# Kernel optimization log

Measured on AMD Instinct MI355X. Metric: run time of the kernel, lower is better.

The kernel has to match this reference:

```python
import jax, jax.numpy as jnp
import numpy as np

HIDDEN = 512
MEM = 512
COMM = 512
N = 8192


def setup_inputs() -> dict:
    key = jax.random.key(0)
    ks = jax.random.split(key, 8)
    in_dim = HIDDEN + MEM
    s = 1.0 / np.sqrt(in_dim)
    return {
        "u": jax.random.normal(ks[0], (N, HIDDEN), dtype=jnp.float32),
        "z": jax.random.normal(ks[1], (N, MEM), dtype=jnp.float32),
        # torch Linear weights have shape (out, in); biases init to 0 per _init_weights
        "Wk": jax.random.normal(ks[2], (COMM, in_dim), dtype=jnp.float32) * s,
        "bk": jnp.zeros((COMM,), dtype=jnp.float32),
        "Wv": jax.random.normal(ks[3], (COMM, in_dim), dtype=jnp.float32) * s,
        "bv": jnp.zeros((COMM,), dtype=jnp.float32),
        "Wq": jax.random.normal(ks[4], (COMM, in_dim), dtype=jnp.float32) * s,
        "bq": jnp.zeros((COMM,), dtype=jnp.float32),
    }


def reference(u, z, Wk, bk, Wv, bv, Wq, bq):
    n = u.shape[0]
    scale = jnp.sqrt(jnp.asarray(Wk.shape[0], dtype=u.dtype))
    s = jnp.concatenate([u, z], axis=-1)              # (N, in_dim)
    keys = s @ Wk.T + bk                              # (N, C)
    values = s @ Wv.T + bv                            # (N, C)
    queries = s @ Wq.T + bq                           # (N, C)
    scores = (queries @ keys.T) / scale               # (N, N)
    eye = jnp.eye(n, dtype=bool)
    scores = jnp.where(eye, -jnp.inf, scores)         # self-mask
    comm_attn = jax.nn.softmax(scores, axis=-1)
    comm_attn = jnp.nan_to_num(comm_attn, nan=0.0)
    m_bar = comm_attn @ values                        # (N, C)
    return (m_bar, comm_attn)
```

## Files before the change

### kernel.cpp

```cpp
#include <hip/hip_runtime.h>
#include <hip/hip_bf16.h>
#include <stdint.h>

#define N_TOK 8192
#define IN_DIM 1024
#define CDIM 512
#define NW 1536

typedef short bf16x8 __attribute__((ext_vector_type(8)));
typedef float f32x4 __attribute__((ext_vector_type(4)));

__device__ __forceinline__ unsigned short f2bf(float f) {
  union { float f; unsigned int u; } x; x.f = f;
  unsigned int u = x.u;
  u += 0x7fffu + ((u >> 16) & 1u);
  return (unsigned short)(u >> 16);
}
__device__ __forceinline__ float bf2f(unsigned short us) {
  union { unsigned int u; float f; } x; x.u = ((unsigned int)us) << 16;
  return x.f;
}

#define GLD16(g, l) __builtin_amdgcn_global_load_lds( \
    (const __attribute__((address_space(1))) void*)(g), \
    (__attribute__((address_space(3))) void*)(l), 16, 0, 0)

__global__ __launch_bounds__(256) void k_convert(
    const float* __restrict__ u, const float* __restrict__ z,
    const float* __restrict__ wk, const float* __restrict__ wv,
    const float* __restrict__ wq,
    ushort* __restrict__ Sb, ushort* __restrict__ Wb) {
  const int S4 = N_TOK * IN_DIM / 4;
  const int W4 = NW * IN_DIM / 4;
  const int total = S4 + W4;
  for (int e = blockIdx.x * blockDim.x + threadIdx.x; e < total;
       e += gridDim.x * blockDim.x) {
    float4 v; ushort* dst;
    if (e < S4) {
      int idx = e << 2; int row = idx >> 10; int col = idx & 1023;
      const float* src = (col < 512) ? (u + row * 512 + col)
                                     : (z + row * 512 + (col - 512));
      v = *(const float4*)src;
      dst = Sb + idx;
    } else {
      int idx = (e - S4) << 2; int row = idx >> 10; int col = idx & 1023;
      const float* base = (row < 512) ? wk : (row < 1024 ? wv : wq);
      v = *(const float4*)(base + (size_t)(row & 511) * 1024 + col);
      dst = Wb + idx;
    }
    ushort4 o;
    o.x = f2bf(v.x); o.y = f2bf(v.y); o.z = f2bf(v.z); o.w = f2bf(v.w);
    *(ushort4*)dst = o;
  }
}

__global__ __launch_bounds__(256) void k_kvq(
    const ushort* __restrict__ Sb, const ushort* __restrict__ Wb,
    const float* __restrict__ bk, const float* __restrict__ bv,
    const float* __restrict__ bq,
    ushort* __restrict__ Kb, ushort* __restrict__ Qb, ushort* __restrict__ VT) {
  __shared__ __align__(16) ushort As[128 * 64];
  __shared__ __align__(16) ushort Bs[128 * 64];
  const int tid = threadIdx.x, lane = tid & 63, w = tid >> 6;
  const int wr = w >> 1, wc = w & 1;
  const int tm = blockIdx.x, tn = blockIdx.y;

  f32x4 acc[4][4];
#pragma unroll
  for (int m = 0; m < 4; m++)
#pragma unroll
    for (int n = 0; n < 4; n++) acc[m][n] = (f32x4){0.f, 0.f, 0.f, 0.f};

  const ushort* ga0 = Sb + (size_t)tm * 128 * IN_DIM;
  const ushort* gb0 = Wb + (size_t)tn * 128 * IN_DIM;

  for (int k0 = 0; k0 < IN_DIM; k0 += 64) {
#pragma unroll
    for (int i = 0; i < 4; i++) {
      int ce = i * 256 + tid;
      int row = ce >> 3, c8 = (ce & 7) << 3;
      GLD16(ga0 + (size_t)row * IN_DIM + k0 + c8, As + ce * 8);
      GLD16(gb0 + (size_t)row * IN_DIM + k0 + c8, Bs + ce * 8);
    }
    __syncthreads();
#pragma unroll
    for (int kb = 0; kb < 2; kb++) {
      bf16x8 af[4], bfr[4];
#pragma unroll
      for (int m = 0; m < 4; m++)
        af[m] = *(const bf16x8*)(As + (wr * 64 + m * 16 + (lane & 15)) * 64 +
                                 kb * 32 + ((lane >> 4) << 3));
#pragma unroll
      for (int n = 0; n < 4; n++)
        bfr[n] = *(const bf16x8*)(Bs + (wc * 64 + n * 16 + (lane & 15)) * 64 +
                                  kb * 32 + ((lane >> 4) << 3));
#pragma unroll
      for (int m = 0; m < 4; m++)
#pragma unroll
        for (int n = 0; n < 4; n++)
          acc[m][n] = __builtin_amdgcn_mfma_f32_16x16x32_bf16(af[m], bfr[n],
                                                              acc[m][n], 0, 0, 0);
    }
    __syncthreads();
  }

  const int region = tn >> 2;
  const int colr = (tn & 3) * 128 + wc * 64;
  const int rbase = tm * 128 + wr * 64;
  const float* bias = (region == 0) ? bk : (region == 1 ? bv : bq);
  if (region == 1) {
#pragma unroll
    for (int m = 0; m < 4; m++) {
      int r0 = rbase + m * 16 + ((lane >> 4) << 2);
#pragma unroll
      for (int n = 0; n < 4; n++) {
        int c = colr + n * 16 + (lane & 15);
        float b = bias[c];
        ushort4 pk;
        pk.x = f2bf(acc[m][n][0] + b);
        pk.y = f2bf(acc[m][n][1] + b);
        pk.z = f2bf(acc[m][n][2] + b);
        pk.w = f2bf(acc[m][n][3] + b);
        *(ushort4*)(VT + (size_t)c * N_TOK + r0) = pk;
      }
    }
  } else {
    ushort* O = (region == 0) ? Kb : Qb;
#pragma unroll
    for (int m = 0; m < 4; m++) {
      int r0 = rbase + m * 16 + ((lane >> 4) << 2);
#pragma unroll
      for (int n = 0; n < 4; n++) {
        int c = colr + n * 16 + (lane & 15);
        float b = bias[c];
#pragma unroll
        for (int rg = 0; rg < 4; rg++)
          O[(size_t)(r0 + rg) * CDIM + c] = f2bf(acc[m][n][rg] + b);
      }
    }
  }
}

__global__ __launch_bounds__(256) void k_scores(
    const ushort* __restrict__ Qb, const ushort* __restrict__ Kb,
    ushort* __restrict__ E, float* __restrict__ rowpart) {
  __shared__ __align__(16) ushort As[128 * 64];
  __shared__ __align__(16) ushort Bs[128 * 64];
  __shared__ float sums[256];
  const int tid = threadIdx.x, lane = tid & 63, w = tid >> 6;
  const int wr = w >> 1, wc = w & 1;
  const int tm = blockIdx.x, tn = blockIdx.y;

  f32x4 acc[4][4];
#pragma unroll
  for (int m = 0; m < 4; m++)
#pragma unroll
    for (int n = 0; n < 4; n++) acc[m][n] = (f32x4){0.f, 0.f, 0.f, 0.f};

  const ushort* ga0 = Qb + (size_t)tm * 128 * CDIM;
  const ushort* gb0 = Kb + (size_t)tn * 128 * CDIM;

  for (int k0 = 0; k0 < CDIM; k0 += 64) {
#pragma unroll
    for (int i = 0; i < 4; i++) {
      int ce = i * 256 + tid;
      int row = ce >> 3, c8 = (ce & 7) << 3;
      GLD16(ga0 + (size_t)row * CDIM + k0 + c8, As + ce * 8);
      GLD16(gb0 + (size_t)row * CDIM + k0 + c8, Bs + ce * 8);
    }
    __syncthreads();
#pragma unroll
    for (int kb = 0; kb < 2; kb++) {
      bf16x8 af[4], bfr[4];
#pragma unroll
      for (int m = 0; m < 4; m++)
        af[m] = *(const bf16x8*)(As + (wr * 64 + m * 16 + (lane & 15)) * 64 +
                                 kb * 32 + ((lane >> 4) << 3));
#pragma unroll
      for (int n = 0; n < 4; n++)
        bfr[n] = *(const bf16x8*)(Bs + (wc * 64 + n * 16 + (lane & 15)) * 64 +
                                  kb * 32 + ((lane >> 4) << 3));
#pragma unroll
      for (int m = 0; m < 4; m++)
#pragma unroll
        for (int n = 0; n < 4; n++)
          acc[m][n] = __builtin_amdgcn_mfma_f32_16x16x32_bf16(af[m], bfr[n],
                                                              acc[m][n], 0, 0, 0);
    }
    __syncthreads();
  }

  const float scale = 0.044194173824159216f;
  float rs[4][4];
#pragma unroll
  for (int m = 0; m < 4; m++)
#pragma unroll
    for (int rg = 0; rg < 4; rg++) rs[m][rg] = 0.f;

#pragma unroll
  for (int m = 0; m < 4; m++) {
    int grow_b = tm * 128 + wr * 64 + m * 16 + ((lane >> 4) << 2);
#pragma unroll
    for (int n = 0; n < 4; n++) {
      int gcol = tn * 128 + wc * 64 + n * 16 + (lane & 15);
#pragma unroll
      for (int rg = 0; rg < 4; rg++) {
        int grow = grow_b + rg;
        float ev = (grow == gcol) ? 0.0f : __expf(acc[m][n][rg] * scale);
        unsigned short evb = f2bf(ev);
        E[(size_t)grow * N_TOK + gcol] = evb;
        rs[m][rg] += bf2f(evb);
      }
    }
  }
#pragma unroll
  for (int m = 0; m < 4; m++)
#pragma unroll
    for (int rg = 0; rg < 4; rg++) {
      float s = rs[m][rg];
      s += __shfl_xor(s, 1);
      s += __shfl_xor(s, 2);
      s += __shfl_xor(s, 4);
      s += __shfl_xor(s, 8);
      rs[m][rg] = s;
    }
  if ((lane & 15) == 0) {
#pragma unroll
    for (int m = 0; m < 4; m++)
#pragma unroll
      for (int rg = 0; rg < 4; rg++)
        sums[wc * 128 + wr * 64 + m * 16 + ((lane >> 4) << 2) + rg] = rs[m][rg];
  }
  __syncthreads();
  if (tid < 128)
    rowpart[(size_t)(tm * 128 + tid) * 64 + tn] = sums[tid] + sums[128 + tid];
}

__global__ __launch_bounds__(256) void k_rcp(const float* __restrict__ rowpart,
                                             float* __restrict__ rcp_l) {
  int row = blockIdx.x * blockDim.x + threadIdx.x;
  if (row < N_TOK) {
    const float4* p = (const float4*)(rowpart + (size_t)row * 64);
    float s = 0.f;
#pragma unroll
    for (int i = 0; i < 16; i++) {
      float4 v = p[i];
      s += v.x + v.y + v.z + v.w;
    }
    rcp_l[row] = 1.0f / s;
  }
}

__global__ __launch_bounds__(256) void k_pv_norm(
    const ushort* __restrict__ E, const ushort* __restrict__ VT,
    const float* __restrict__ rcp_l, float* __restrict__ mbar,
    float* __restrict__ attn) {
  __shared__ __align__(16) ushort As[128 * 64];
  __shared__ __align__(16) ushort Bs[64 * 64];
  const int tid = threadIdx.x, lane = tid & 63, w = tid >> 6;
  const int wr = w >> 1, wc = w & 1;
  const int tm = blockIdx.x, tn = blockIdx.y;

  f32x4 acc[4][2];
#pragma unroll
  for (int m = 0; m < 4; m++)
#pragma unroll
    for (int n = 0; n < 2; n++) acc[m][n] = (f32x4){0.f, 0.f, 0.f, 0.f};

  const ushort* ga0 = E + (size_t)tm * 128 * N_TOK;
  const ushort* gb0 = VT + (size_t)tn * 64 * N_TOK;
  const int kw_lo = tn << 10;
  const int kw_hi = kw_lo + 1024;

  for (int k0 = 0; k0 < N_TOK; k0 += 64) {
#pragma unroll
    for (int i = 0; i < 4; i++) {
      int ce = i * 256 + tid;
      int row = ce >> 3, c8 = (ce & 7) << 3;
      GLD16(ga0 + (size_t)row * N_TOK + k0 + c8, As + ce * 8);
    }
#pragma unroll
    for (int i = 0; i < 2; i++) {
      int ce = i * 256 + tid;
      int row = ce >> 3, c8 = (ce & 7) << 3;
      GLD16(gb0 + (size_t)row * N_TOK + k0 + c8, Bs + ce * 8);
    }
    __syncthreads();
#pragma unroll
    for (int kb = 0; kb < 2; kb++) {
      bf16x8 af[4], bfr[2];
#pragma unroll
      for (int m = 0; m < 4; m++)
        af[m] = *(const bf16x8*)(As + (wr * 64 + m * 16 + (lane & 15)) * 64 +
                                 kb * 32 + ((lane >> 4) << 3));
#pragma unroll
      for (int n = 0; n < 2; n++)
        bfr[n] = *(const bf16x8*)(Bs + (wc * 32 + n * 16 + (lane & 15)) * 64 +
                                  kb * 32 + ((lane >> 4) << 3));
#pragma unroll
      for (int m = 0; m < 4; m++)
#pragma unroll
        for (int n = 0; n < 2; n++)
          acc[m][n] = __builtin_amdgcn_mfma_f32_16x16x32_bf16(af[m], bfr[n],
                                                              acc[m][n], 0, 0, 0);
    }

    if (attn != nullptr && k0 >= kw_lo && k0 < kw_hi) {
#pragma unroll
      for (int p = 0; p < 4; p++) {
        int ce = p * 256 + tid;
        int row = ce >> 3;
        int c8 = (ce & 7) << 3;
        int grow = tm * 128 + row;
        float rl = rcp_l[grow];
        uint4 ev = *(const uint4*)(E + ((size_t)grow << 13) + k0 + c8);
        float4 o0, o1;
        o0.x = bf2f((unsigned short)(ev.x & 0xffffu)) * rl;
        o0.y = bf2f((unsigned short)(ev.x >> 16)) * rl;
        o0.z = bf2f((unsigned short)(ev.y & 0xffffu)) * rl;
        o0.w = bf2f((unsigned short)(ev.y >> 16)) * rl;
        o1.x = bf2f((unsigned short)(ev.z & 0xffffu)) * rl;
        o1.y = bf2f((unsigned short)(ev.z >> 16)) * rl;
        o1.z = bf2f((unsigned short)(ev.w & 0xffffu)) * rl;
        o1.w = bf2f((unsigned short)(ev.w >> 16)) * rl;
        float* op = attn + ((size_t)grow << 13) + k0 + c8;
        *(float4*)op = o0;
        *(float4*)(op + 4) = o1;
      }
    }
    __syncthreads();
  }

#pragma unroll
  for (int m = 0; m < 4; m++) {
    int r0 = tm * 128 + wr * 64 + m * 16 + ((lane >> 4) << 2);
#pragma unroll
    for (int n = 0; n < 2; n++) {
      int c = tn * 64 + wc * 32 + n * 16 + (lane & 15);
#pragma unroll
      for (int rg = 0; rg < 4; rg++)
        mbar[(size_t)(r0 + rg) * CDIM + c] = acc[m][n][rg] * rcp_l[r0 + rg];
    }
  }
}

__global__ __launch_bounds__(256) void k_norm(
    const ushort* __restrict__ E, float* __restrict__ attn,
    const float* __restrict__ rcp_l, int row0, int nrows) {
  const int units = nrows << 10;
  for (int uidx = blockIdx.x * blockDim.x + threadIdx.x; uidx < units;
       uidx += gridDim.x * blockDim.x) {
    int row = row0 + (uidx >> 10);
    int c8 = (uidx & 1023) << 3;
    const float rl = rcp_l[row];
    uint4 ev = *(const uint4*)(E + ((size_t)row << 13) + c8);
    float4 o0, o1;
    o0.x = bf2f((unsigned short)(ev.x & 0xffffu)) * rl;
    o0.y = bf2f((unsigned short)(ev.x >> 16)) * rl;
    o0.z = bf2f((unsigned short)(ev.y & 0xffffu)) * rl;
    o0.w = bf2f((unsigned short)(ev.y >> 16)) * rl;
    o1.x = bf2f((unsigned short)(ev.z & 0xffffu)) * rl;
    o1.y = bf2f((unsigned short)(ev.z >> 16)) * rl;
    o1.z = bf2f((unsigned short)(ev.w & 0xffffu)) * rl;
    o1.w = bf2f((unsigned short)(ev.w >> 16)) * rl;
    float* op = attn + ((size_t)row << 13) + c8;
    *(float4*)op = o0;
    *(float4*)(op + 4) = o1;
  }
}

__global__ __launch_bounds__(256) void k_lastrow(
    const ushort* __restrict__ E, float* __restrict__ attn,
    const float* __restrict__ rcp_l) {
  const int row = N_TOK - 1;
  const int t = threadIdx.x;
  const float rl = rcp_l[row];
  const uint4* src = (const uint4*)(E + ((size_t)row << 13)) + t * 4;
  uint4 rr[4] = {src[0], src[1], src[2], src[3]};
  __syncthreads();
  float* dst = attn + ((size_t)row << 13) + t * 32;
#pragma unroll
  for (int q = 0; q < 4; q++) {
    float4 o0, o1;
    o0.x = bf2f((unsigned short)(rr[q].x & 0xffffu)) * rl;
    o0.y = bf2f((unsigned short)(rr[q].x >> 16)) * rl;
    o0.z = bf2f((unsigned short)(rr[q].y & 0xffffu)) * rl;
    o0.w = bf2f((unsigned short)(rr[q].y >> 16)) * rl;
    o1.x = bf2f((unsigned short)(rr[q].z & 0xffffu)) * rl;
    o1.y = bf2f((unsigned short)(rr[q].z >> 16)) * rl;
    o1.z = bf2f((unsigned short)(rr[q].w & 0xffffu)) * rl;
    o1.w = bf2f((unsigned short)(rr[q].w >> 16)) * rl;
    *(float4*)(dst + q * 8) = o0;
    *(float4*)(dst + q * 8 + 4) = o1;
  }
}

extern "C" void kernel_launch(void* const* d_in, const int* in_sizes, int n_in,
                              void* d_out, int out_size, void* d_ws,
                              size_t ws_size, hipStream_t stream) {
  const float* u  = (const float*)d_in[0];
  const float* z  = (const float*)d_in[1];
  const float* Wk = (const float*)d_in[2];
  const float* bk = (const float*)d_in[3];
  const float* Wv = (const float*)d_in[4];
  const float* bv = (const float*)d_in[5];
  const float* Wq = (const float*)d_in[6];
  const float* bq = (const float*)d_in[7];

  float* mbar = (float*)d_out;
  float* attn = (float*)d_out + (size_t)N_TOK * CDIM;

  char* ws = (char*)d_ws;
  ushort* Kb      = (ushort*)(ws + 0);
  ushort* Qb      = (ushort*)(ws + 8388608);
  ushort* VT      = (ushort*)(ws + 16777216);
  float*  rcp_l   = (float*)(ws + 25165824);
  float*  rowpart = (float*)(ws + 25198592);
  ushort* Sb      = (ushort*)(ws + 27295744);
  ushort* Wb      = (ushort*)(ws + 44072960);
  const size_t E_WS_OFF = 27295744;
  const size_t REQ = E_WS_OFF + 134217728;
  const bool ws_mode = (ws_size >= REQ);
  ushort* E = ws_mode ? (ushort*)(ws + E_WS_OFF)
                      : (ushort*)((char*)attn + 134217728);

  k_convert<<<dim3(2048), dim3(256), 0, stream>>>(u, z, Wk, Wv, Wq, Sb, Wb);
  k_kvq<<<dim3(64, 12), dim3(256), 0, stream>>>(Sb, Wb, bk, bv, bq, Kb, Qb, VT);
  k_scores<<<dim3(64, 64), dim3(256), 0, stream>>>(Qb, Kb, E, rowpart);
  k_rcp<<<dim3(32), dim3(256), 0, stream>>>(rowpart, rcp_l);
  k_pv_norm<<<dim3(64, 8), dim3(256), 0, stream>>>(E, VT, rcp_l, mbar,
                                                   ws_mode ? attn : nullptr);

  if (!ws_mode) {
    static const int ph[] = {0, 4096, 6144, 7168, 7680, 7936, 8064, 8128,
                             8160, 8176, 8184, 8188, 8190, 8191};
    for (int p = 0; p + 1 < (int)(sizeof(ph) / sizeof(ph[0])); ++p) {
      int a = ph[p], b = ph[p + 1];
      int units = (b - a) << 10;
      int blocks = (units + 255) / 256;
      if (blocks > 2048) blocks = 2048;
      k_norm<<<dim3(blocks), dim3(256), 0, stream>>>(E, attn, rcp_l, a, b - a);
    }
    k_lastrow<<<dim3(1), dim3(256), 0, stream>>>(E, attn, rcp_l);
  }
}
```

Baseline: 398.8 us.

## Split PV GEMM over K into two halves and swizzle LDS tiles

The PV kernel's grid gains a z dimension that splits the 8192-long reduction into two halves, raising the block count from 512 to 1024 so more CUs stay busy. Partial sums go to mbar and to a workspace buffer that aliases the no-longer-needed K buffer, and a new reduce kernel adds them and applies the row normalization. LDS tiles also use an XOR swizzle on the 16-byte chunk index to cut bank conflicts on MFMA fragment loads. The cost is an extra launch and an extra read and write of the partial outputs.

```diff
diff --git a/kernel.cpp b/kernel.cpp
--- a/kernel.cpp
+++ b/kernel.cpp
@@ -253,13 +253,14 @@
 
 __global__ __launch_bounds__(256) void k_pv_norm(
     const ushort* __restrict__ E, const ushort* __restrict__ VT,
-    const float* __restrict__ rcp_l, float* __restrict__ mbar,
-    float* __restrict__ attn) {
+    const float* __restrict__ rcp_l, float* __restrict__ part0,
+    float* __restrict__ part1, float* __restrict__ attn) {
   __shared__ __align__(16) ushort As[128 * 64];
   __shared__ __align__(16) ushort Bs[64 * 64];
   const int tid = threadIdx.x, lane = tid & 63, w = tid >> 6;
   const int wr = w >> 1, wc = w & 1;
-  const int tm = blockIdx.x, tn = blockIdx.y;
+  const int tm = blockIdx.x, tn = blockIdx.y, kz = blockIdx.z;
+  const int kbase = kz << 12;
 
   f32x4 acc[4][2];
 #pragma unroll
@@ -269,34 +270,38 @@
 
   const ushort* ga0 = E + (size_t)tm * 128 * N_TOK;
   const ushort* gb0 = VT + (size_t)tn * 64 * N_TOK;
-  const int kw_lo = tn << 10;
-  const int kw_hi = kw_lo + 1024;
-
-  for (int k0 = 0; k0 < N_TOK; k0 += 64) {
+  const int kw_lo = kbase + (tn << 9);
+  const int kw_hi = kw_lo + 512;
+  const int sx = lane & 7;
+
+  for (int k0 = kbase; k0 < kbase + 4096; k0 += 64) {
 #pragma unroll
     for (int i = 0; i < 4; i++) {
       int ce = i * 256 + tid;
-      int row = ce >> 3, c8 = (ce & 7) << 3;
+      int row = ce >> 3;
+      int c8 = ((ce & 7) ^ (row & 7)) << 3;
       GLD16(ga0 + (size_t)row * N_TOK + k0 + c8, As + ce * 8);
     }
 #pragma unroll
     for (int i = 0; i < 2; i++) {
       int ce = i * 256 + tid;
-      int row = ce >> 3, c8 = (ce & 7) << 3;
+      int row = ce >> 3;
+      int c8 = ((ce & 7) ^ (row & 7)) << 3;
       GLD16(gb0 + (size_t)row * N_TOK + k0 + c8, Bs + ce * 8);
     }
     __syncthreads();
 #pragma unroll
     for (int kb = 0; kb < 2; kb++) {
+      const int chunk = ((kb * 4 + (lane >> 4)) ^ sx) << 3;
       bf16x8 af[4], bfr[2];
 #pragma unroll
       for (int m = 0; m < 4; m++)
         af[m] = *(const bf16x8*)(As + (wr * 64 + m * 16 + (lane & 15)) * 64 +
-                                 kb * 32 + ((lane >> 4) << 3));
+                                 chunk);
 #pragma unroll
       for (int n = 0; n < 2; n++)
         bfr[n] = *(const bf16x8*)(Bs + (wc * 32 + n * 16 + (lane & 15)) * 64 +
-                                  kb * 32 + ((lane >> 4) << 3));
+                                  chunk);
 #pragma unroll
       for (int m = 0; m < 4; m++)
 #pragma unroll
@@ -331,6 +336,7 @@
     __syncthreads();
   }
 
+  float* P = kz ? part1 : part0;
 #pragma unroll
   for (int m = 0; m < 4; m++) {
     int r0 = tm * 128 + wr * 64 + m * 16 + ((lane >> 4) << 2);
@@ -339,8 +345,25 @@
       int c = tn * 64 + wc * 32 + n * 16 + (lane & 15);
 #pragma unroll
       for (int rg = 0; rg < 4; rg++)
-        mbar[(size_t)(r0 + rg) * CDIM + c] = acc[m][n][rg] * rcp_l[r0 + rg];
-    }
+        P[(size_t)(r0 + rg) * CDIM + c] = acc[m][n][rg];
+    }
+  }
+}
+
+__global__ __launch_bounds__(256) void k_reduce_split(
+    float* __restrict__ part0, const float* __restrict__ part1,
+    const float* __restrict__ rcp_l) {
+  int idx4 = blockIdx.x * blockDim.x + threadIdx.x;
+  const int T4 = N_TOK * CDIM / 4;
+  if (idx4 < T4) {
+    int row = idx4 >> 7;
+    float rl = rcp_l[row];
+    float4 a = ((const float4*)part0)[idx4];
+    float4 b = ((const float4*)part1)[idx4];
+    float4 o;
+    o.x = (a.x + b.x) * rl; o.y = (a.y + b.y) * rl;
+    o.z = (a.z + b.z) * rl; o.w = (a.w + b.w) * rl;
+    ((float4*)part0)[idx4] = o;
   }
 }
 
@@ -418,6 +441,7 @@
   float*  rowpart = (float*)(ws + 25198592);
   ushort* Sb      = (ushort*)(ws + 27295744);
   ushort* Wb      = (ushort*)(ws + 44072960);
+  float*  part1   = (float*)(ws + 0);
   const size_t E_WS_OFF = 27295744;
   const size_t REQ = E_WS_OFF + 134217728;
   const bool ws_mode = (ws_size >= REQ);
@@ -428,8 +452,9 @@
   k_kvq<<<dim3(64, 12), dim3(256), 0, stream>>>(Sb, Wb, bk, bv, bq, Kb, Qb, VT);
   k_scores<<<dim3(64, 64), dim3(256), 0, stream>>>(Qb, Kb, E, rowpart);
   k_rcp<<<dim3(32), dim3(256), 0, stream>>>(rowpart, rcp_l);
-  k_pv_norm<<<dim3(64, 8), dim3(256), 0, stream>>>(E, VT, rcp_l, mbar,
-                                                   ws_mode ? attn : nullptr);
+  k_pv_norm<<<dim3(64, 8, 2), dim3(256), 0, stream>>>(
+      E, VT, rcp_l, mbar, part1, ws_mode ? attn : nullptr);
+  k_reduce_split<<<dim3(4096), dim3(256), 0, stream>>>(mbar, part1, rcp_l);
 
   if (!ws_mode) {
     static const int ph[] = {0, 4096, 6144, 7168, 7680, 7936, 8064, 8128,
```

Measured after the change: 401.4 us. About the same (+0.6%).
